# Kernel optimization log

Measured on AMD Instinct MI355X. Metric: run time of the kernel, lower is better.

Reference implementation:

```python
import jax, jax.numpy as jnp
import numpy as np

TOPK = 4  # constructor default topk=4


def setup_inputs() -> dict:
    key = jax.random.key(0)
    k_x, k_a, k_b, k_w, k_bias = jax.random.split(key, 5)
    b, s, h, j, a, r = 4, 2048, 2048, 2048, 64, 16
    x = jax.random.normal(k_x, (b, s, h), dtype=jnp.float32)
    A = jax.random.normal(k_a, (a, r, h), dtype=jnp.float32) * 0.02   # adapter down-proj bank
    B = jax.random.normal(k_b, (a, j, r), dtype=jnp.float32) * 0.02   # adapter up-proj bank
    W = jax.random.normal(k_w, (j, h), dtype=jnp.float32) * 0.02      # base Linear weight
    bias = jax.random.normal(k_bias, (j,), dtype=jnp.float32) * 0.02  # base Linear bias
    return {"x": x, "A": A, "B": B, "W": W, "bias": bias}


def reference(x, A, B, W, bias):
    # vecs: per-adapter low-rank projections of each token. [b,s,a,r]
    vecs = jnp.einsum('arh,bsh->bsar', A, x)
    # routing score = L2 norm over rank dim. [b,s,a]
    arrows = jnp.linalg.norm(vecs, axis=-1)
    # top-k adapters per token -> uniform 1/topk routing weights (scatter of a constant,
    # so no gradient flows through the routing weights, matching torch semantics).
    _, idx = jax.lax.top_k(arrows, TOPK)                     # [b,s,topk]
    routes = jax.nn.one_hot(idx, arrows.shape[-1], dtype=x.dtype).sum(-2) / TOPK  # [b,s,a]
    # weighted combine of selected adapter vecs. [b,s,r]
    v = jnp.einsum('bsa,bsar->bsr', routes, vecs)
    # delta = (routes-weighted B) applied to v; contract over a then r without
    # materializing the [b,s,j,r] intermediate. [b,s,j]
    delta = jnp.einsum('bsa,ajr,bsr->bsj', routes, B, v)
    base = jnp.einsum('bsh,jh->bsj', x, W) + bias
    return base + delta
```

## Files before the change

### kernel.cpp

```cpp
#include <hip/hip_runtime.h>
#include <hip/hip_bf16.h>
#include <stdint.h>

#define TOKENS 8192
#define H 2048
#define JDIM 2048
#define NADAPT 64
#define RANK 16
#define KG 1024
#define KTOT 3072
#define NT2 48
#define NT1 64

typedef __bf16 v8bf __attribute__((ext_vector_type(8)));
typedef float v4f __attribute__((ext_vector_type(4)));
typedef unsigned short us8 __attribute__((ext_vector_type(8)));
typedef unsigned short us4 __attribute__((ext_vector_type(4)));

__device__ __forceinline__ unsigned short f2bf(float f) {
  union { __bf16 b; unsigned short u; } c; c.b = (__bf16)f; return c.u;
}
__device__ __forceinline__ float bf2f(unsigned short u) {
  union { unsigned int u; float f; } c; c.u = ((unsigned int)u) << 16; return c.f;
}

__device__ __forceinline__ us8 pack8(float4 a, float4 b) {
  us8 r;
  r[0]=f2bf(a.x); r[1]=f2bf(a.y); r[2]=f2bf(a.z); r[3]=f2bf(a.w);
  r[4]=f2bf(b.x); r[5]=f2bf(b.y); r[6]=f2bf(b.z); r[7]=f2bf(b.w);
  return r;
}

__device__ __forceinline__ void split8(float4 a, float4 b, us8& h, us8& l) {
  float v[8] = {a.x, a.y, a.z, a.w, b.x, b.y, b.z, b.w};
  #pragma unroll
  for (int i = 0; i < 8; ++i) {
    h[i] = f2bf(v[i]);
    l[i] = f2bf(v[i] - bf2f(h[i]));
  }
}

__global__ void cast_x_split_kernel(const float* __restrict__ x,
                                    unsigned short* __restrict__ XG,
                                    unsigned short* __restrict__ XLO) {
  int idx = blockIdx.x * 256 + threadIdx.x;
  int row = idx >> 8;
  int cg  = idx & 255;
  const float4* s = (const float4*)(x + ((size_t)row << 11) + ((size_t)cg << 3));
  float4 a = s[0], b = s[1];
  us8 h, l;
  split8(a, b, h, l);
  *(us8*)(XG  + (size_t)row * KTOT + ((size_t)cg << 3)) = h;
  *(us8*)(XLO + (size_t)row * H    + ((size_t)cg << 3)) = l;
}

__global__ void cast_a_split_kernel(const float* __restrict__ A,
                                    unsigned short* __restrict__ Ahi,
                                    unsigned short* __restrict__ Alo) {
  int idx = blockIdx.x * 256 + threadIdx.x;
  int row = idx >> 8;
  int cg  = idx & 255;
  const float4* s = (const float4*)(A + ((size_t)row << 11) + ((size_t)cg << 3));
  float4 a = s[0], b = s[1];
  us8 h, l;
  split8(a, b, h, l);
  *(us8*)(Ahi + (size_t)row * H + ((size_t)cg << 3)) = h;
  *(us8*)(Alo + (size_t)row * H + ((size_t)cg << 3)) = l;
}

__global__ void cast2048_kernel(const float* __restrict__ src,
                                unsigned short* __restrict__ dst, int dstld) {
  int idx = blockIdx.x * 256 + threadIdx.x;
  int row = idx >> 8;
  int cg  = idx & 255;
  const float4* s = (const float4*)(src + ((size_t)row << 11) + ((size_t)cg << 3));
  float4 a = s[0], b = s[1];
  *(us8*)(dst + (size_t)row * dstld + ((size_t)cg << 3)) = pack8(a, b);
}

__global__ void cast_b_kernel(const float* __restrict__ Bsrc,
                              unsigned short* __restrict__ WB) {
  int idx = blockIdx.x * 256 + threadIdx.x;
  int a = idx >> 11, j = idx & 2047;
  const float4* s = (const float4*)(Bsrc + (((size_t)a << 11) + j) * RANK);
  float4 f0 = s[0], f1 = s[1], f2 = s[2], f3 = s[3];
  us8* d = (us8*)(WB + (size_t)j * KTOT + H + a * RANK);
  d[0] = pack8(f0, f1);
  d[1] = pack8(f2, f3);
}

__global__ void route_kernel(const float* __restrict__ vecs,
                             unsigned short* __restrict__ XG) {
  __shared__ float vsh[4][16];
  int wave = threadIdx.x >> 6, lane = threadIdx.x & 63;
  int t = blockIdx.x * 4 + wave;
  const float* vrow = vecs + (size_t)t * KG;
  const float4* vp = (const float4*)(vrow + lane * RANK);
  float4 q0 = vp[0], q1 = vp[1], q2 = vp[2], q3 = vp[3];
  float ss = q0.x*q0.x + q0.y*q0.y + q0.z*q0.z + q0.w*q0.w
           + q1.x*q1.x + q1.y*q1.y + q1.z*q1.z + q1.w*q1.w
           + q2.x*q2.x + q2.y*q2.y + q2.z*q2.z + q2.w*q2.w
           + q3.x*q3.x + q3.y*q3.y + q3.z*q3.z + q3.w*q3.w;
  float arr = ss;
  int sel[4];
  #pragma unroll
  for (int k = 0; k < 4; ++k) {
    float m = arr; int mi = lane;
    #pragma unroll
    for (int o = 32; o > 0; o >>= 1) {
      float om = __shfl_xor(m, o);
      int oi  = __shfl_xor(mi, o);
      if (om > m || (om == m && oi < mi)) { m = om; mi = oi; }
    }
    sel[k] = mi;
    if (lane == mi) arr = -3.0e38f;
  }
  if (lane < 16) {
    float s = vrow[sel[0]*RANK + lane] + vrow[sel[1]*RANK + lane]
            + vrow[sel[2]*RANK + lane] + vrow[sel[3]*RANK + lane];
    vsh[wave][lane] = 0.0625f * s;
  }
  __syncthreads();
  bool on = (lane == sel[0]) | (lane == sel[1]) | (lane == sel[2]) | (lane == sel[3]);
  us8 lo, hi;
  #pragma unroll
  for (int r = 0; r < 8; ++r) lo[r] = on ? f2bf(vsh[wave][r])     : (unsigned short)0;
  #pragma unroll
  for (int r = 0; r < 8; ++r) hi[r] = on ? f2bf(vsh[wave][r + 8]) : (unsigned short)0;
  us8* d = (us8*)(XG + (size_t)t * KTOT + H + lane * RANK);
  d[0] = lo; d[1] = hi;
}

__device__ __forceinline__ void gload_lds16(const void* gsrc, void* ldst) {
  __builtin_amdgcn_global_load_lds(
      (const __attribute__((address_space(1))) unsigned int*)gsrc,
      (__attribute__((address_space(3))) unsigned int*)ldst, 16, 0, 0);
}

#define BAR()  asm volatile("s_waitcnt lgkmcnt(0)\n\ts_barrier" ::: "memory")
#define BARO() asm volatile("s_barrier" ::: "memory")
#define VM4() asm volatile("s_waitcnt vmcnt(4)" ::: "memory")
#define VM6() asm volatile("s_waitcnt vmcnt(6)" ::: "memory")
#define VM8() asm volatile("s_waitcnt vmcnt(8)" ::: "memory")
#define P1() __builtin_amdgcn_s_setprio(1)
#define P0() __builtin_amdgcn_s_setprio(0)

#define MM1(mi, xf, bv) do {                                                   \
  acc[mi][0] = __builtin_amdgcn_mfma_f32_16x16x32_bf16(xf, bv[0], acc[mi][0], 0, 0, 0); \
  acc[mi][1] = __builtin_amdgcn_mfma_f32_16x16x32_bf16(xf, bv[1], acc[mi][1], 0, 0, 0); \
  acc[mi][2] = __builtin_amdgcn_mfma_f32_16x16x32_bf16(xf, bv[2], acc[mi][2], 0, 0, 0); \
  acc[mi][3] = __builtin_amdgcn_mfma_f32_16x16x32_bf16(xf, bv[3], acc[mi][3], 0, 0, 0); \
} while (0)

#define S_XH1(B, kel) gload_lds16(XhB + (size_t)srow * KTOT + (kel) + scol, (B) + tid*16)
#define S_XH2(B, kel) gload_lds16(XhB + (size_t)(srow + 128) * KTOT + (kel) + scol, (B) + 8192 + tid*16)
#define S_XL1(B, kel) gload_lds16(XlB + (size_t)srow * H + (kel) + scol, (B) + 16384 + tid*16)
#define S_XL2(B, kel) gload_lds16(XlB + (size_t)(srow + 128) * H + (kel) + scol, (B) + 24576 + tid*16)
#define S_AH1(B, kel) gload_lds16(AhB + (size_t)srow * H + (kel) + scol, (B) + 32768 + tid*16)
#define S_AL1(B, kel) gload_lds16(AlB + (size_t)srow * H + (kel) + scol, (B) + 40960 + tid*16)

__global__ __launch_bounds__(512, 1) void gemm1_8ph_kernel(
    const unsigned short* __restrict__ Xhi,
    const unsigned short* __restrict__ Xlo,
    const unsigned short* __restrict__ Ahi,
    const unsigned short* __restrict__ Alo,
    float* __restrict__ C) {
  __shared__ char Ls[147456];
  const int tid = threadIdx.x;
  const int lane = tid & 63, wid = tid >> 6;
  const int wr = wid >> 1, wc = wid & 1;
  const int rA = lane & 15, grp = lane >> 4;
  const int grpx = (grp ^ ((rA >> 1) & 3)) << 4;

  const int bid = blockIdx.x;
  const int g = bid & 7, r = bid >> 3;
  const int bm = g * 4 + (r & 3), bn = r >> 2;

  const unsigned short* XhB = Xhi + (size_t)(bm * 256) * KTOT;
  const unsigned short* XlB = Xlo + (size_t)(bm * 256) * H;
  const unsigned short* AhB = Ahi + (size_t)(bn * 128) * H;
  const unsigned short* AlB = Alo + (size_t)(bn * 128) * H;

  const int srow = tid >> 2;
  const int scol = ((tid & 3) ^ ((tid >> 3) & 3)) << 3;

  const int abyte = (wr * 64 + rA) * 64 + grpx;
  const int bbyte = (wc * 64 + rA) * 64 + grpx;

  char* bufA = Ls;
  char* bufB = Ls + 49152;
  char* bufC = Ls + 98304;

  v4f acc[4][4];
  #pragma unroll
  for (int i = 0; i < 4; ++i)
    #pragma unroll
    for (int j = 0; j < 4; ++j)
      acc[i][j] = (v4f){0.f, 0.f, 0.f, 0.f};
  v8bf xh[4], xl[4], ah[4], al[4];

  S_XH1(bufA, 0); S_XH2(bufA, 0); S_AH1(bufA, 0); S_XL1(bufA, 0); S_XL2(bufA, 0); S_AL1(bufA, 0);
  S_XH1(bufB, 32); S_XH2(bufB, 32); S_AH1(bufB, 32); S_XL1(bufB, 32); S_XL2(bufB, 32); S_AL1(bufB, 32);
  VM8(); BAR();
  #pragma unroll
  for (int i = 0; i < 4; ++i) xh[i] = *(const v8bf*)(bufA + abyte + i * 1024);
  #pragma unroll
  for (int j = 0; j < 4; ++j) ah[j] = *(const v8bf*)(bufA + 32768 + bbyte + j * 1024);

  #pragma unroll 1
  for (int t = 0; t < NT1; ++t) {
    const int kel = (t + 2 < NT1 ? t + 2 : NT1 - 1) * 32;
    P1(); MM1(0, xh[0], ah); MM1(1, xh[1], ah); MM1(2, xh[2], ah); MM1(3, xh[3], ah); P0();
    #pragma unroll
    for (int j = 0; j < 4; ++j) al[j] = *(const v8bf*)(bufA + 40960 + bbyte + j * 1024);
    S_XH1(bufC, kel); S_XH2(bufC, kel);
    VM4(); BARO();
    P1(); MM1(0, xh[0], al); MM1(1, xh[1], al); MM1(2, xh[2], al); MM1(3, xh[3], al); P0();
    #pragma unroll
    for (int i = 0; i < 4; ++i) xl[i] = *(const v8bf*)(bufA + 16384 + abyte + i * 1024);
    S_AH1(bufC, kel); S_XL1(bufC, kel);
    VM4(); BARO();
    P1(); MM1(0, xl[0], ah); MM1(1, xl[1], ah); MM1(2, xl[2], ah); MM1(3, xl[3], ah); P0();
    #pragma unroll
    for (int i = 0; i < 4; ++i) xh[i] = *(const v8bf*)(bufB + abyte + i * 1024);
    #pragma unroll
    for (int j = 0; j < 4; ++j) ah[j] = *(const v8bf*)(bufB + 32768 + bbyte + j * 1024);
    S_XL2(bufC, kel); S_AL1(bufC, kel);
    VM4(); BARO();
    char* tmp = bufA; bufA = bufB; bufB = bufC; bufC = tmp;
  }

  const int row0 = bm * 256 + wr * 64 + (grp << 2);
  const int col0 = bn * 128 + wc * 64 + rA;
  #pragma unroll
  for (int mi = 0; mi < 4; ++mi)
    #pragma unroll
    for (int j = 0; j < 4; ++j)
      #pragma unroll
      for (int q = 0; q < 4; ++q)
        C[(size_t)(row0 + mi * 16 + q) * KG + col0 + j * 16] = acc[mi][j][q];
}

#define STAGE(regionUS, panel, kelem) do {                                        \
  gload_lds16((panel) + aoff0 + (kelem), (char*)(regionUS) + tid * 16);           \
  gload_lds16((panel) + aoff1 + (kelem), (char*)(regionUS) + 8192 + tid * 16);    \
} while (0)

#define PH2A(AFC, RAn, AFN, STG) do {                                             \
  P1();                                                                           \
  _Pragma("unroll")                                                               \
  for (int i = 0; i < 4; ++i)                                                     \
    _Pragma("unroll")                                                             \
    for (int j = 0; j < 4; ++j)                                                   \
      acc[i][j] = __builtin_amdgcn_mfma_f32_16x16x32_bf16(                        \
          AFC[i], bfr[j], acc[i][j], 0, 0, 0);                                    \
  P0();                                                                           \
  _Pragma("unroll")                                                               \
  for (int i = 0; i < 4; ++i)                                                     \
    AFN[i] = *(const v8bf*)((const char*)(RAn) + abyte + (4 + i) * 1024);         \
  STG;                                                                            \
  VM6(); BARO();                                                                  \
} while (0)

#define PH2B(AFC, RBn, RAn, AFN, STG) do {                                        \
  P1();                                                                           \
  _Pragma("unroll")                                                               \
  for (int i = 0; i < 4; ++i)                                                     \
    _Pragma("unroll")                                                             \
    for (int j = 0; j < 4; ++j)                                                   \
      acc[4 + i][j] = __builtin_amdgcn_mfma_f32_16x16x32_bf16(                    \
          AFC[i], bfr[j], acc[4 + i][j], 0, 0, 0);                                \
  P0();                                                                           \
  _Pragma("unroll")                                                               \
  for (int j = 0; j < 4; ++j)                                                     \
    bfr[j] = *(const v8bf*)((const char*)(RBn) + bbyte + j * 1024);               \
  _Pragma("unroll")                                                               \
  for (int i = 0; i < 4; ++i)                                                     \
    AFN[i] = *(const v8bf*)((const char*)(RAn) + abyte + i * 1024);               \
  STG;                                                                            \
  VM6(); BARO();                                                                  \
} while (0)

__global__ __launch_bounds__(512, 1) void gemm2_8ph_kernel(
    const unsigned short* __restrict__ Xg, const unsigned short* __restrict__ Wb,
    float* __restrict__ C, const float* __restrict__ bias) {
  __shared__ unsigned short lds[65536];
  const int tid = threadIdx.x;
  const int lane = tid & 63, wid = tid >> 6;
  const int wr = wid >> 2, wc = wid & 3;
  const int rA = lane & 15, grp = lane >> 4;
  const int grpx = (grp ^ ((rA >> 1) & 3)) << 4;

  const int bid = blockIdx.x;
  const int g = bid & 7, r = bid >> 3;
  const int bm = g * 4 + (r & 3), bn = r >> 2;

  const unsigned short* Ap = Xg + (size_t)(bm * 256) * KTOT;
  const unsigned short* Bp = Wb + (size_t)(bn * 256) * KTOT;

  const int srow = tid >> 2;
  const int scol = ((tid & 3) ^ ((tid >> 3) & 3)) << 3;
  const size_t aoff0 = (size_t)srow * KTOT + scol;
  const size_t aoff1 = (size_t)(srow + 128) * KTOT + scol;

  unsigned short* A0k0 = lds;
  unsigned short* A0k1 = lds + 8192;
  unsigned short* B0k0 = lds + 16384;
  unsigned short* B0k1 = lds + 24576;
  unsigned short* A1k0 = lds + 32768;
  unsigned short* A1k1 = lds + 40960;
  unsigned short* B1k0 = lds + 49152;
  unsigned short* B1k1 = lds + 57344;

  const int abyte = (wr * 128 + rA) * 64 + grpx;
  const int bbyte = (wc * 64 + rA) * 64 + grpx;

  v4f acc[8][4];
  #pragma unroll
  for (int i = 0; i < 8; ++i)
    #pragma unroll
    for (int j = 0; j < 4; ++j)
      acc[i][j] = (v4f){0.f, 0.f, 0.f, 0.f};
  v8bf afA[4], afB[4], bfr[4];

  STAGE(A0k0, Ap, 0);
  STAGE(B0k0, Bp, 0);
  STAGE(A0k1, Ap, 32);
  STAGE(B0k1, Bp, 32);
  STAGE(A1k0, Ap, 64);
  STAGE(B1k0, Bp, 64);
  VM8();
  BAR();
  #pragma unroll
  for (int i = 0; i < 4; ++i) afA[i] = *(const v8bf*)((const char*)A0k0 + abyte + i * 1024);
  #pragma unroll
  for (int j = 0; j < 4; ++j) bfr[j] = *(const v8bf*)((const char*)B0k0 + bbyte + j * 1024);

  #pragma unroll 1
  for (int t = 0; t < NT2; t += 2) {
    const int k1a = (t + 1) * 64 + 32;
    const int k0a = (t + 2 < NT2 ? t + 2 : NT2 - 1) * 64;
    const int k1b = (t + 2 < NT2 ? t + 2 : NT2 - 1) * 64 + 32;
    const int k0b = (t + 3 < NT2 ? t + 3 : NT2 - 1) * 64;
    PH2A(afA, A0k0, afB, STAGE(A1k1, Ap, k1a));
    PH2B(afB, B0k1, A0k1, afA, STAGE(B1k1, Bp, k1a));
    PH2A(afA, A0k1, afB, STAGE(A0k0, Ap, k0a));
    PH2B(afB, B1k0, A1k0, afA, STAGE(B0k0, Bp, k0a));
    PH2A(afA, A1k0, afB, STAGE(A0k1, Ap, k1b));
    PH2B(afB, B1k1, A1k1, afA, STAGE(B0k1, Bp, k1b));
    PH2A(afA, A1k1, afB, STAGE(A1k0, Ap, k0b));
    PH2B(afB, B0k0, A0k0, afA, STAGE(B1k0, Bp, k0b));
  }

  const int row0 = bm * 256 + wr * 128 + (grp << 2);
  const int col0 = bn * 256 + wc * 64 + rA;
  float bv[4];
  #pragma unroll
  for (int j = 0; j < 4; ++j) bv[j] = bias[col0 + j * 16];
  #pragma unroll
  for (int mi = 0; mi < 8; ++mi)
    #pragma unroll
    for (int j = 0; j < 4; ++j)
      #pragma unroll
      for (int q = 0; q < 4; ++q)
        C[(size_t)(row0 + mi * 16 + q) * JDIM + col0 + j * 16] = acc[mi][j][q] + bv[j];
}

extern "C" void kernel_launch(void* const* d_in, const int* in_sizes, int n_in,
                              void* d_out, int out_size, void* d_ws, size_t ws_size,
                              hipStream_t stream) {
  const float* x    = (const float*)d_in[0];
  const float* A    = (const float*)d_in[1];
  const float* Bb   = (const float*)d_in[2];
  const float* W    = (const float*)d_in[3];
  const float* bias = (const float*)d_in[4];
  float* out = (float*)d_out;

  char* ws = (char*)d_ws;
  unsigned short* XG  = (unsigned short*)ws;
  unsigned short* WB  = (unsigned short*)(ws + (size_t)48 * 1024 * 1024);
  unsigned short* Ahi = (unsigned short*)(ws + (size_t)60 * 1024 * 1024);
  unsigned short* Alo = (unsigned short*)(ws + (size_t)64 * 1024 * 1024);
  float* vecs         = (float*)d_out;
  unsigned short* XLO = (unsigned short*)((char*)d_out + (size_t)32 * 1024 * 1024);

  cast_x_split_kernel<<<TOKENS, 256, 0, stream>>>(x, XG, XLO);
  cast_a_split_kernel<<<KG, 256, 0, stream>>>(A, Ahi, Alo);
  cast2048_kernel<<<JDIM, 256, 0, stream>>>(W, WB, KTOT);
  cast_b_kernel<<<512, 256, 0, stream>>>(Bb, WB);

  gemm1_8ph_kernel<<<256, 512, 0, stream>>>(XG, XLO, Ahi, Alo, vecs);

  route_kernel<<<TOKENS / 4, 256, 0, stream>>>(vecs, XG);

  gemm2_8ph_kernel<<<256, 512, 0, stream>>>(XG, WB, out, bias);
}
```

Before: 213.1 us.

## Fuse cast kernels and rework GEMM pipelines with double-buffered fragments and fewer barriers

The four separate cast launches become one cast kernel that picks its work by block-index range, which removes launch overhead. In gemm1 the loop is unrolled by two with ping-pong adapter-fragment registers, and one wait-plus-barrier per tile is dropped. In gemm2 the B fragments are double-buffered so they load during the odd phase, and the barrier runs only on even phases, halving the sync points. The prologue barrier now waits for all outstanding loads. Fewer barriers add risk of LDS read/write races and raise register pressure.

```diff
diff --git a/kernel.cpp b/kernel.cpp
--- a/kernel.cpp
+++ b/kernel.cpp
@@ -40,53 +40,47 @@
   }
 }
 
-__global__ void cast_x_split_kernel(const float* __restrict__ x,
-                                    unsigned short* __restrict__ XG,
-                                    unsigned short* __restrict__ XLO) {
-  int idx = blockIdx.x * 256 + threadIdx.x;
-  int row = idx >> 8;
-  int cg  = idx & 255;
-  const float4* s = (const float4*)(x + ((size_t)row << 11) + ((size_t)cg << 3));
-  float4 a = s[0], b = s[1];
-  us8 h, l;
-  split8(a, b, h, l);
-  *(us8*)(XG  + (size_t)row * KTOT + ((size_t)cg << 3)) = h;
-  *(us8*)(XLO + (size_t)row * H    + ((size_t)cg << 3)) = l;
-}
-
-__global__ void cast_a_split_kernel(const float* __restrict__ A,
-                                    unsigned short* __restrict__ Ahi,
-                                    unsigned short* __restrict__ Alo) {
-  int idx = blockIdx.x * 256 + threadIdx.x;
-  int row = idx >> 8;
-  int cg  = idx & 255;
-  const float4* s = (const float4*)(A + ((size_t)row << 11) + ((size_t)cg << 3));
-  float4 a = s[0], b = s[1];
-  us8 h, l;
-  split8(a, b, h, l);
-  *(us8*)(Ahi + (size_t)row * H + ((size_t)cg << 3)) = h;
-  *(us8*)(Alo + (size_t)row * H + ((size_t)cg << 3)) = l;
-}
-
-__global__ void cast2048_kernel(const float* __restrict__ src,
-                                unsigned short* __restrict__ dst, int dstld) {
-  int idx = blockIdx.x * 256 + threadIdx.x;
-  int row = idx >> 8;
-  int cg  = idx & 255;
-  const float4* s = (const float4*)(src + ((size_t)row << 11) + ((size_t)cg << 3));
-  float4 a = s[0], b = s[1];
-  *(us8*)(dst + (size_t)row * dstld + ((size_t)cg << 3)) = pack8(a, b);
-}
-
-__global__ void cast_b_kernel(const float* __restrict__ Bsrc,
-                              unsigned short* __restrict__ WB) {
-  int idx = blockIdx.x * 256 + threadIdx.x;
-  int a = idx >> 11, j = idx & 2047;
-  const float4* s = (const float4*)(Bsrc + (((size_t)a << 11) + j) * RANK);
-  float4 f0 = s[0], f1 = s[1], f2 = s[2], f3 = s[3];
-  us8* d = (us8*)(WB + (size_t)j * KTOT + H + a * RANK);
-  d[0] = pack8(f0, f1);
-  d[1] = pack8(f2, f3);
+__global__ void cast_all_kernel(const float* __restrict__ x,
+                                const float* __restrict__ A,
+                                const float* __restrict__ W,
+                                const float* __restrict__ Bsrc,
+                                unsigned short* __restrict__ XG,
+                                unsigned short* __restrict__ XLO,
+                                unsigned short* __restrict__ Ahi,
+                                unsigned short* __restrict__ Alo,
+                                unsigned short* __restrict__ WB) {
+  int bid = blockIdx.x;
+  int cg = threadIdx.x;
+  if (bid < TOKENS) {
+    int row = bid;
+    const float4* s = (const float4*)(x + ((size_t)row << 11) + ((size_t)cg << 3));
+    float4 a = s[0], b = s[1];
+    us8 h, l;
+    split8(a, b, h, l);
+    *(us8*)(XG  + (size_t)row * KTOT + ((size_t)cg << 3)) = h;
+    *(us8*)(XLO + (size_t)row * H    + ((size_t)cg << 3)) = l;
+  } else if (bid < TOKENS + KG) {
+    int row = bid - TOKENS;
+    const float4* s = (const float4*)(A + ((size_t)row << 11) + ((size_t)cg << 3));
+    float4 a = s[0], b = s[1];
+    us8 h, l;
+    split8(a, b, h, l);
+    *(us8*)(Ahi + ((size_t)row << 11) + ((size_t)cg << 3)) = h;
+    *(us8*)(Alo + ((size_t)row << 11) + ((size_t)cg << 3)) = l;
+  } else if (bid < TOKENS + KG + JDIM) {
+    int row = bid - TOKENS - KG;
+    const float4* s = (const float4*)(W + ((size_t)row << 11) + ((size_t)cg << 3));
+    float4 a = s[0], b = s[1];
+    *(us8*)(WB + (size_t)row * KTOT + ((size_t)cg << 3)) = pack8(a, b);
+  } else {
+    int idx = (bid - TOKENS - KG - JDIM) * 256 + cg;
+    int a = idx >> 11, j = idx & 2047;
+    const float4* s = (const float4*)(Bsrc + (((size_t)a << 11) + j) * RANK);
+    float4 f0 = s[0], f1 = s[1], f2 = s[2], f3 = s[3];
+    us8* d = (us8*)(WB + (size_t)j * KTOT + H + a * RANK);
+    d[0] = pack8(f0, f1);
+    d[1] = pack8(f2, f3);
+  }
 }
 
 __global__ void route_kernel(const float* __restrict__ vecs,
@@ -137,11 +131,9 @@
       (__attribute__((address_space(3))) unsigned int*)ldst, 16, 0, 0);
 }
 
-#define BAR()  asm volatile("s_waitcnt lgkmcnt(0)\n\ts_barrier" ::: "memory")
+#define BAR()  asm volatile("s_waitcnt vmcnt(0) lgkmcnt(0)\n\ts_barrier" ::: "memory")
 #define BARO() asm volatile("s_barrier" ::: "memory")
 #define VM4() asm volatile("s_waitcnt vmcnt(4)" ::: "memory")
-#define VM6() asm volatile("s_waitcnt vmcnt(6)" ::: "memory")
-#define VM8() asm volatile("s_waitcnt vmcnt(8)" ::: "memory")
 #define P1() __builtin_amdgcn_s_setprio(1)
 #define P0() __builtin_amdgcn_s_setprio(0)
 
@@ -158,6 +150,32 @@
 #define S_XL2(B, kel) gload_lds16(XlB + (size_t)(srow + 128) * H + (kel) + scol, (B) + 24576 + tid*16)
 #define S_AH1(B, kel) gload_lds16(AhB + (size_t)srow * H + (kel) + scol, (B) + 32768 + tid*16)
 #define S_AL1(B, kel) gload_lds16(AlB + (size_t)srow * H + (kel) + scol, (B) + 40960 + tid*16)
+
+#define TILE1(AHC, AHN, kel) do {                                              \
+                    \
+  P1(); MM1(0, xh[0], AHC); MM1(1, xh[1], AHC);                                \
+        MM1(2, xh[2], AHC); MM1(3, xh[3], AHC); P0();                          \
+  _Pragma("unroll")                                                            \
+  for (int j = 0; j < 4; ++j) al[j] = *(const v8bf*)(bufA + 40960 + bbyte + j * 1024); \
+  S_XH1(bufC, kel); S_XH2(bufC, kel);                                          \
+                             \
+  P1(); MM1(0, xh[0], al); MM1(1, xh[1], al);                                  \
+        MM1(2, xh[2], al); MM1(3, xh[3], al); P0();                            \
+  _Pragma("unroll")                                                            \
+  for (int i = 0; i < 4; ++i) xl[i] = *(const v8bf*)(bufA + 16384 + abyte + i * 1024); \
+  S_AH1(bufC, kel); S_XL1(bufC, kel);                                          \
+  VM4(); BARO();                                                               \
+                 \
+  P1(); MM1(0, xl[0], AHC); MM1(1, xl[1], AHC);                                \
+        MM1(2, xl[2], AHC); MM1(3, xl[3], AHC); P0();                          \
+  _Pragma("unroll")                                                            \
+  for (int i = 0; i < 4; ++i) xh[i] = *(const v8bf*)(bufB + abyte + i * 1024); \
+  _Pragma("unroll")                                                            \
+  for (int j = 0; j < 4; ++j) AHN[j] = *(const v8bf*)(bufB + 32768 + bbyte + j * 1024); \
+  S_XL2(bufC, kel); S_AL1(bufC, kel);                                          \
+  VM4(); BARO();                                                               \
+  { char* tmp_ = bufA; bufA = bufB; bufB = bufC; bufC = tmp_; }                \
+} while (0)
 
 __global__ __launch_bounds__(512, 1) void gemm1_8ph_kernel(
     const unsigned short* __restrict__ Xhi,
@@ -197,37 +215,22 @@
     #pragma unroll
     for (int j = 0; j < 4; ++j)
       acc[i][j] = (v4f){0.f, 0.f, 0.f, 0.f};
-  v8bf xh[4], xl[4], ah[4], al[4];
+  v8bf xh[4], xl[4], al[4], ahA[4], ahB_[4];
 
   S_XH1(bufA, 0); S_XH2(bufA, 0); S_AH1(bufA, 0); S_XL1(bufA, 0); S_XL2(bufA, 0); S_AL1(bufA, 0);
   S_XH1(bufB, 32); S_XH2(bufB, 32); S_AH1(bufB, 32); S_XL1(bufB, 32); S_XL2(bufB, 32); S_AL1(bufB, 32);
-  VM8(); BAR();
+  BAR();
   #pragma unroll
   for (int i = 0; i < 4; ++i) xh[i] = *(const v8bf*)(bufA + abyte + i * 1024);
   #pragma unroll
-  for (int j = 0; j < 4; ++j) ah[j] = *(const v8bf*)(bufA + 32768 + bbyte + j * 1024);
+  for (int j = 0; j < 4; ++j) ahA[j] = *(const v8bf*)(bufA + 32768 + bbyte + j * 1024);
 
   #pragma unroll 1
-  for (int t = 0; t < NT1; ++t) {
-    const int kel = (t + 2 < NT1 ? t + 2 : NT1 - 1) * 32;
-    P1(); MM1(0, xh[0], ah); MM1(1, xh[1], ah); MM1(2, xh[2], ah); MM1(3, xh[3], ah); P0();
-    #pragma unroll
-    for (int j = 0; j < 4; ++j) al[j] = *(const v8bf*)(bufA + 40960 + bbyte + j * 1024);
-    S_XH1(bufC, kel); S_XH2(bufC, kel);
-    VM4(); BARO();
-    P1(); MM1(0, xh[0], al); MM1(1, xh[1], al); MM1(2, xh[2], al); MM1(3, xh[3], al); P0();
-    #pragma unroll
-    for (int i = 0; i < 4; ++i) xl[i] = *(const v8bf*)(bufA + 16384 + abyte + i * 1024);
-    S_AH1(bufC, kel); S_XL1(bufC, kel);
-    VM4(); BARO();
-    P1(); MM1(0, xl[0], ah); MM1(1, xl[1], ah); MM1(2, xl[2], ah); MM1(3, xl[3], ah); P0();
-    #pragma unroll
-    for (int i = 0; i < 4; ++i) xh[i] = *(const v8bf*)(bufB + abyte + i * 1024);
-    #pragma unroll
-    for (int j = 0; j < 4; ++j) ah[j] = *(const v8bf*)(bufB + 32768 + bbyte + j * 1024);
-    S_XL2(bufC, kel); S_AL1(bufC, kel);
-    VM4(); BARO();
-    char* tmp = bufA; bufA = bufB; bufB = bufC; bufC = tmp;
+  for (int t = 0; t < NT1; t += 2) {
+    const int ka = (t + 2 < NT1 ? t + 2 : NT1 - 1) * 32;
+    const int kb = (t + 3 < NT1 ? t + 3 : NT1 - 1) * 32;
+    TILE1(ahA, ahB_, ka);
+    TILE1(ahB_, ahA, kb);
   }
 
   const int row0 = bm * 256 + wr * 64 + (grp << 2);
@@ -246,39 +249,38 @@
   gload_lds16((panel) + aoff1 + (kelem), (char*)(regionUS) + 8192 + tid * 16);    \
 } while (0)
 
-#define PH2A(AFC, RAn, AFN, STG) do {                                             \
+#define PHO(AFC, BFC, RA, AFN, RB, BFN, STG) do {                                 \
   P1();                                                                           \
   _Pragma("unroll")                                                               \
   for (int i = 0; i < 4; ++i)                                                     \
     _Pragma("unroll")                                                             \
     for (int j = 0; j < 4; ++j)                                                   \
       acc[i][j] = __builtin_amdgcn_mfma_f32_16x16x32_bf16(                        \
-          AFC[i], bfr[j], acc[i][j], 0, 0, 0);                                    \
+          AFC[i], BFC[j], acc[i][j], 0, 0, 0);                                    \
   P0();                                                                           \
   _Pragma("unroll")                                                               \
   for (int i = 0; i < 4; ++i)                                                     \
-    AFN[i] = *(const v8bf*)((const char*)(RAn) + abyte + (4 + i) * 1024);         \
+    AFN[i] = *(const v8bf*)((const char*)(RA) + abyte + (4 + i) * 1024);          \
+  _Pragma("unroll")                                                               \
+  for (int j = 0; j < 4; ++j)                                                     \
+    BFN[j] = *(const v8bf*)((const char*)(RB) + bbyte + j * 1024);                \
   STG;                                                                            \
-  VM6(); BARO();                                                                  \
-} while (0)
-
-#define PH2B(AFC, RBn, RAn, AFN, STG) do {                                        \
+} while (0)
+
+#define PHE(AFC, BFC, RA, AFN, STG) do {                                          \
   P1();                                                                           \
   _Pragma("unroll")                                                               \
   for (int i = 0; i < 4; ++i)                                                     \
     _Pragma("unroll")                                                             \
     for (int j = 0; j < 4; ++j)                                                   \
       acc[4 + i][j] = __builtin_amdgcn_mfma_f32_16x16x32_bf16(                    \
-          AFC[i], bfr[j], acc[4 + i][j], 0, 0, 0);                                \
+          AFC[i], BFC[j], acc[4 + i][j], 0, 0, 0);                                \
   P0();                                                                           \
   _Pragma("unroll")                                                               \
-  for (int j = 0; j < 4; ++j)                                                     \
-    bfr[j] = *(const v8bf*)((const char*)(RBn) + bbyte + j * 1024);               \
-  _Pragma("unroll")                                                               \
   for (int i = 0; i < 4; ++i)                                                     \
-    AFN[i] = *(const v8bf*)((const char*)(RAn) + abyte + i * 1024);               \
+    AFN[i] = *(const v8bf*)((const char*)(RA) + abyte + i * 1024);                \
   STG;                                                                            \
-  VM6(); BARO();                                                                  \
+  VM4(); BARO();                                                                  \
 } while (0)
 
 __global__ __launch_bounds__(512, 1) void gemm2_8ph_kernel(
@@ -321,7 +323,7 @@
     #pragma unroll
     for (int j = 0; j < 4; ++j)
       acc[i][j] = (v4f){0.f, 0.f, 0.f, 0.f};
-  v8bf afA[4], afB[4], bfr[4];
+  v8bf afA[4], afB[4], bfrA[4], bfrB[4];
 
   STAGE(A0k0, Ap, 0);
   STAGE(B0k0, Bp, 0);
@@ -329,12 +331,11 @@
   STAGE(B0k1, Bp, 32);
   STAGE(A1k0, Ap, 64);
   STAGE(B1k0, Bp, 64);
-  VM8();
   BAR();
   #pragma unroll
   for (int i = 0; i < 4; ++i) afA[i] = *(const v8bf*)((const char*)A0k0 + abyte + i * 1024);
   #pragma unroll
-  for (int j = 0; j < 4; ++j) bfr[j] = *(const v8bf*)((const char*)B0k0 + bbyte + j * 1024);
+  for (int j = 0; j < 4; ++j) bfrA[j] = *(const v8bf*)((const char*)B0k0 + bbyte + j * 1024);
 
   #pragma unroll 1
   for (int t = 0; t < NT2; t += 2) {
@@ -342,14 +343,14 @@
     const int k0a = (t + 2 < NT2 ? t + 2 : NT2 - 1) * 64;
     const int k1b = (t + 2 < NT2 ? t + 2 : NT2 - 1) * 64 + 32;
     const int k0b = (t + 3 < NT2 ? t + 3 : NT2 - 1) * 64;
-    PH2A(afA, A0k0, afB, STAGE(A1k1, Ap, k1a));
-    PH2B(afB, B0k1, A0k1, afA, STAGE(B1k1, Bp, k1a));
-    PH2A(afA, A0k1, afB, STAGE(A0k0, Ap, k0a));
-    PH2B(afB, B1k0, A1k0, afA, STAGE(B0k0, Bp, k0a));
-    PH2A(afA, A1k0, afB, STAGE(A0k1, Ap, k1b));
-    PH2B(afB, B1k1, A1k1, afA, STAGE(B0k1, Bp, k1b));
-    PH2A(afA, A1k1, afB, STAGE(A1k0, Ap, k0b));
-    PH2B(afB, B0k0, A0k0, afA, STAGE(B1k0, Bp, k0b));
+    PHO(afA, bfrA, A0k0, afB, B0k1, bfrB, STAGE(A1k1, Ap, k1a));
+    PHE(afB, bfrA, A0k1, afA, STAGE(B1k1, Bp, k1a));
+    PHO(afA, bfrB, A0k1, afB, B1k0, bfrA, STAGE(A0k0, Ap, k0a));
+    PHE(afB, bfrB, A1k0, afA, STAGE(B0k0, Bp, k0a));
+    PHO(afA, bfrA, A1k0, afB, B1k1, bfrB, STAGE(A0k1, Ap, k1b));
+    PHE(afB, bfrA, A1k1, afA, STAGE(B0k1, Bp, k1b));
+    PHO(afA, bfrB, A1k1, afB, B0k0, bfrA, STAGE(A1k0, Ap, k0b));
+    PHE(afB, bfrB, A0k0, afA, STAGE(B1k0, Bp, k0b));
   }
 
   const int row0 = bm * 256 + wr * 128 + (grp << 2);
@@ -384,10 +385,8 @@
   float* vecs         = (float*)d_out;
   unsigned short* XLO = (unsigned short*)((char*)d_out + (size_t)32 * 1024 * 1024);
 
-  cast_x_split_kernel<<<TOKENS, 256, 0, stream>>>(x, XG, XLO);
-  cast_a_split_kernel<<<KG, 256, 0, stream>>>(A, Ahi, Alo);
-  cast2048_kernel<<<JDIM, 256, 0, stream>>>(W, WB, KTOT);
-  cast_b_kernel<<<512, 256, 0, stream>>>(Bb, WB);
+  cast_all_kernel<<<TOKENS + KG + JDIM + 512, 256, 0, stream>>>(
+      x, A, W, Bb, XG, XLO, Ahi, Alo, WB);
 
   gemm1_8ph_kernel<<<256, 512, 0, stream>>>(XG, XLO, Ahi, Alo, vecs);
 
```

Measured after the change: 212.0 us. Within noise of the previous version (-0.5%).
